# Optimization experiments

Measured on AMD Instinct MI355X. Metric: run time of the kernel, lower is better.

## Reference

```python
import jax, jax.numpy as jnp
import numpy as np

L = 4          # n_layers
D = 1024       # d_model
QD = D // 4    # quat_dim
B = 8
T = 2048
VOCAB = 32000
NUM_CLASSES = 1000
EPS_LN = 1e-5
EPS_FILT = 1e-8


def layer_norm(x, w, b):
    m = x.mean(-1, keepdims=True)
    v = ((x - m) ** 2).mean(-1, keepdims=True)
    return (x - m) / jnp.sqrt(v + EPS_LN) * w + b


def spectral_filter(k, alpha):
    # F(k) = exp(i * alpha * arctan(ln(|k| + eps))); k complex [B,T,4,QD]
    phase = alpha * jnp.arctan(jnp.log(jnp.abs(k) + EPS_FILT))
    return jnp.cos(phase) + 1j * jnp.sin(phase)


def hamilton(q1, q2):
    # q1, q2: [..., 4, QD] with components [w, x, y, z] along dim -2
    w1, x1, y1, z1 = q1[..., 0, :], q1[..., 1, :], q1[..., 2, :], q1[..., 3, :]
    w2, x2, y2, z2 = q2[..., 0, :], q2[..., 1, :], q2[..., 2, :], q2[..., 3, :]
    w = w1 * w2 - x1 * x2 - y1 * y2 - z1 * z2
    x = w1 * x2 + x1 * w2 + y1 * z2 - z1 * y2
    y = w1 * y2 - x1 * z2 + y1 * w2 + z1 * x2
    z = w1 * z2 + x1 * y2 - y1 * x2 + z1 * w2
    return jnp.stack([w, x, y, z], axis=-2)


def setup_inputs() -> dict:
    key = jax.random.key(0)
    ks = jax.random.split(key, 16)
    f32 = jnp.float32
    inp = {
        "tokens": jax.random.randint(ks[0], (B, T), 0, VOCAB),
        "embed": jax.random.normal(ks[1], (VOCAB, D), f32) * 0.02,
        "pos": jax.random.normal(ks[2], (1, T, D), f32) * 0.02,
        "Wq": jax.random.normal(ks[3], (L, D, D), f32) * 0.02,
        "bq": jnp.zeros((L, D), f32),
        "Wr": jax.random.normal(ks[4], (L, D, D), f32) * 0.02,
        "br": jnp.zeros((L, D), f32),
        "Wh": jax.random.normal(ks[5], (L, D, D), f32) * 0.02,
        "bh": jnp.zeros((L, D), f32),
        "alpha": jnp.full((L, QD), 0.1, f32) + 0.01 * jax.random.normal(ks[6], (L, QD), f32),
        "sp_ln_w": jnp.ones((L, D), f32),
        "sp_ln_b": jnp.zeros((L, D), f32),
        "gate": jnp.ones((L, QD), f32) + 0.01 * jax.random.normal(ks[7], (L, QD), f32),
        "rot": jnp.broadcast_to(jnp.eye(4, dtype=f32), (L, 4, 4)) + 0.01 * jax.random.normal(ks[8], (L, 4, 4), f32),
        "out_ln_w": jnp.ones((L, D), f32),
        "out_ln_b": jnp.zeros((L, D), f32),
        "cls_ln_w": jnp.ones((D,), f32),
        "cls_ln_b": jnp.zeros((D,), f32),
        "cls_W": jax.random.normal(ks[9], (NUM_CLASSES, D), f32) * 0.02,
        "cls_b": jnp.zeros((NUM_CLASSES,), f32),
    }
    return inp


def reference(tokens, embed, pos, Wq, bq, Wr, br, Wh, bh, alpha,
              sp_ln_w, sp_ln_b, gate, rot, out_ln_w, out_ln_b,
              cls_ln_w, cls_ln_b, cls_W, cls_b):
    x = embed[tokens] + pos[:, :T, :]           # [B,T,D]; dropout is identity in eval
    for l in range(L):
        residual = x
        # --- SpectralInterference ---
        Q = (x @ Wq[l].T + bq[l]).reshape(B, T, 4, QD)
        R = (x @ Wr[l].T + br[l]).reshape(B, T, 4, QD)
        H = (x @ Wh[l].T + bh[l]).reshape(B, T, 4, QD)
        Qs = jnp.fft.fft(Q, axis=1)
        Rs = jnp.fft.fft(R, axis=1)
        Qf = Qs * spectral_filter(Qs, alpha[l])
        Rf = Rs * spectral_filter(Rs, alpha[l])
        inter = jnp.fft.ifft(Qf * jnp.conj(Rf), axis=1).real   # [B,T,4,QD]
        out_q = hamilton(inter, H)
        x = layer_norm(out_q.reshape(B, T, D), sp_ln_w[l], sp_ln_b[l])
        # --- HamiltonianEvolution ---
        xq = x.reshape(B, T, 4, QD)
        xs = jnp.fft.fft(xq, axis=1) * gate[l]                  # gate broadcasts over [B,T,4,QD]
        xf = jnp.fft.ifft(xs, axis=1).real
        xr = jnp.einsum('btkd,jk->btjd', xf, rot[l])            # SO(4) rotation on quat axis
        x = layer_norm(xr.reshape(B, T, D) + residual, out_ln_w[l], out_ln_b[l])
    pooled = x.mean(axis=1)                                     # [B,D]
    h = layer_norm(pooled, cls_ln_w, cls_ln_b)
    return h @ cls_W.T + cls_b                                  # [B,NUM_CLASSES]
```

## Files before the change

kernel.cpp:

```cpp
#include <hip/hip_runtime.h>

typedef signed char I8;
typedef __attribute__((ext_vector_type(4))) int i32x4;
typedef __attribute__((ext_vector_type(4))) float f32x4;

#define B_   8
#define T_   2048
#define D_   1024
#define QD_  256
#define L_   4
#define M_   (B_ * T_)
#define NCLS_ 1000
#define DD_  (D_ * D_)

__device__ __forceinline__ float fixf(float v) {
  unsigned u = __float_as_uint(v);
  return ((u & 0x7F800000u) == 0x7F800000u) ? 0.f : v;
}
__device__ __forceinline__ void glds16(const void* g, void* l) {
  __builtin_amdgcn_global_load_lds((const __attribute__((address_space(1))) void*)g,
                                   (__attribute__((address_space(3))) void*)l, 16, 0, 0);
}
__device__ __forceinline__ int clampi(int q) { return q < -128 ? -128 : (q > 127 ? 127 : q); }
__device__ __forceinline__ void quant2(float v, float inv, int& qh, int& ql) {
  const float t = v * inv;
  int h = clampi((int)rintf(t));
  const float r = t - (float)h;
  int l = clampi((int)rintf(r * 256.f));
  qh = h; ql = l;
}
__device__ __forceinline__ void breduce2(float& a, float& b, float* buf) {
#pragma unroll
  for (int off = 32; off > 0; off >>= 1) { a += __shfl_down(a, off); b += __shfl_down(b, off); }
  const int lane = threadIdx.x & 63, w = threadIdx.x >> 6;
  __syncthreads();
  if (lane == 0) { buf[w] = a; buf[4 + w] = b; }
  __syncthreads();
  a = buf[0] + buf[1] + buf[2] + buf[3];
  b = buf[4] + buf[5] + buf[6] + buf[7];
}
__device__ __forceinline__ float bmaxall(float a, float* buf) {
#pragma unroll
  for (int off = 32; off > 0; off >>= 1) a = fmaxf(a, __shfl_down(a, off));
  const int lane = threadIdx.x & 63, w = threadIdx.x >> 6;
  __syncthreads();
  if (lane == 0) buf[w] = a;
  __syncthreads();
  return fmaxf(fmaxf(buf[0], buf[1]), fmaxf(buf[2], buf[3]));
}

__global__ __launch_bounds__(256) void wsplitq_k(const float* __restrict__ Wq,
                                                 const float* __restrict__ Wr,
                                                 const float* __restrict__ Wh,
                                                 I8* __restrict__ hi, I8* __restrict__ lo,
                                                 float* __restrict__ sw) {
  __shared__ float red[4];
  const int sec = blockIdx.x >> 10;
  const int n = blockIdx.x & 1023;
  const float* w = (sec == 0) ? Wq : (sec == 1) ? Wr : Wh;
  const int c = threadIdx.x * 4;
  const float4 v = *(const float4*)(w + (size_t)n * D_ + c);
  const float vv[4] = {v.x, v.y, v.z, v.w};
  float mx = fmaxf(fmaxf(fabsf(v.x), fabsf(v.y)), fmaxf(fabsf(v.z), fabsf(v.w)));
  mx = bmaxall(mx, red);
  const float s = fmaxf(mx, 1e-30f) * (1.f / 127.f);
  if (threadIdx.x == 0) sw[sec * D_ + n] = s;
  const float inv = 127.f / fmaxf(mx, 1e-30f);
  unsigned ph = 0, pl = 0;
#pragma unroll
  for (int j = 0; j < 4; j++) {
    int qh, ql;
    quant2(vv[j], inv, qh, ql);
    ph |= ((unsigned)(unsigned char)(I8)qh) << (8 * j);
    pl |= ((unsigned)(unsigned char)(I8)ql) << (8 * j);
  }
  const size_t o = (size_t)sec * DD_ + (size_t)n * D_ + c;
  *(unsigned*)(hi + o) = ph;
  *(unsigned*)(lo + o) = pl;
}

__global__ __launch_bounds__(256) void embedq_k(const int* __restrict__ tok,
                                                const float* __restrict__ emb,
                                                const float* __restrict__ pos,
                                                I8* __restrict__ xh, I8* __restrict__ xl,
                                                float* __restrict__ sx) {
  __shared__ float red[4];
  const int m = blockIdx.x;
  const int t = m & (T_ - 1);
  const int tk = tok[m];
  const int c = threadIdx.x * 4;
  const float* e = emb + (size_t)tk * D_ + c;
  const float* p = pos + (size_t)t * D_ + c;
  float v[4];
  float mx = 0.f;
#pragma unroll
  for (int i = 0; i < 4; i++) { v[i] = e[i] + p[i]; mx = fmaxf(mx, fabsf(v[i])); }
  mx = bmaxall(mx, red);
  const float s = fmaxf(mx, 1e-30f) * (1.f / 127.f);
  if (threadIdx.x == 0) sx[m] = s;
  const float inv = 127.f / fmaxf(mx, 1e-30f);
  unsigned ph = 0, pl = 0;
#pragma unroll
  for (int i = 0; i < 4; i++) {
    int qh, ql;
    quant2(v[i], inv, qh, ql);
    ph |= ((unsigned)(unsigned char)(I8)qh) << (8 * i);
    pl |= ((unsigned)(unsigned char)(I8)ql) << (8 * i);
  }
  const size_t o = (size_t)m * D_ + c;
  *(unsigned*)(xh + o) = ph;
  *(unsigned*)(xl + o) = pl;
}

__global__ __launch_bounds__(256, 2) void gemm3q_k(const I8* __restrict__ Ahi,
                                                   const I8* __restrict__ Alo,
                                                   const I8* __restrict__ Whi,
                                                   const I8* __restrict__ Wlo,
                                                   const float* __restrict__ sx,
                                                   const float* __restrict__ sw,
                                                   const float* __restrict__ bq,
                                                   const float* __restrict__ br,
                                                   const float* __restrict__ bh,
                                                   float* __restrict__ outQ,
                                                   float* __restrict__ outR,
                                                   float* __restrict__ outH) {
  __shared__ __align__(16) I8 lds[32768];
  char* sbase = (char*)lds;
  const int tid = threadIdx.x;
  const int lane = tid & 63;
  const int wave = tid >> 6;
  const int wr = wave >> 1, wc = wave & 1;
  const int sec = blockIdx.x >> 3;
  const int n0 = (blockIdx.x & 7) * 128;
  const int m0 = blockIdx.y * 128;
  const I8* Bhi = Whi + (size_t)sec * DD_;
  const I8* Blo = Wlo + (size_t)sec * DD_;
  const float* bias = (sec == 0) ? bq : (sec == 1) ? br : bh;
  float* out = (sec == 0) ? outQ : (sec == 1) ? outR : outH;
  const bool TR = sec < 2;

  i32x4 aHH[4][4], aX[4][4];
#pragma unroll
  for (int i = 0; i < 4; i++)
#pragma unroll
    for (int j = 0; j < 4; j++) { aHH[i][j] = (i32x4){0, 0, 0, 0}; aX[i][j] = (i32x4){0, 0, 0, 0}; }

  const int lrow = tid >> 2;
  const int lcolb = (tid & 3) * 16;
  const char* gah = (const char*)Ahi + (size_t)(m0 + lrow) * D_ + lcolb;
  const char* gal = (const char*)Alo + (size_t)(m0 + lrow) * D_ + lcolb;
  const char* gbh = (const char*)Bhi + (size_t)(n0 + lrow) * D_ + lcolb;
  const char* gbl = (const char*)Blo + (size_t)(n0 + lrow) * D_ + lcolb;
  char* s0 = sbase + tid * 16;

  const int koff = (lane >> 4) * 16;
  const int mA = (wr * 64 + (lane & 15)) * 64;
  const int nB = (wc * 64 + (lane & 15)) * 64;

  for (int kk = 0; kk < 1024; kk += 64) {
    __syncthreads();
    glds16(gah, s0);
    glds16(gah + 64 * D_, s0 + 4096);
    glds16(gal, s0 + 8192);
    glds16(gal + 64 * D_, s0 + 12288);
    glds16(gbh, s0 + 16384);
    glds16(gbh + 64 * D_, s0 + 20480);
    glds16(gbl, s0 + 24576);
    glds16(gbl + 64 * D_, s0 + 28672);
    gah += 64; gal += 64; gbh += 64; gbl += 64;
    __syncthreads();
    i32x4 ah[4], al[4], bh2[4], bl2[4];
#pragma unroll
    for (int i = 0; i < 4; i++) {
      const char* pa = sbase + mA + i * 1024 + koff;
      ah[i] = *(const i32x4*)pa;
      al[i] = *(const i32x4*)(pa + 8192);
    }
#pragma unroll
    for (int j = 0; j < 4; j++) {
      const char* pb = sbase + 16384 + nB + j * 1024 + koff;
      bh2[j] = *(const i32x4*)pb;
      bl2[j] = *(const i32x4*)(pb + 8192);
    }
#pragma unroll
    for (int i = 0; i < 4; i++)
#pragma unroll
      for (int j = 0; j < 4; j++) {
        aHH[i][j] = __builtin_amdgcn_mfma_i32_16x16x64_i8(ah[i], bh2[j], aHH[i][j], 0, 0, 0);
        aX[i][j]  = __builtin_amdgcn_mfma_i32_16x16x64_i8(ah[i], bl2[j], aX[i][j], 0, 0, 0);
        aX[i][j]  = __builtin_amdgcn_mfma_i32_16x16x64_i8(al[i], bh2[j], aX[i][j], 0, 0, 0);
      }
  }

#pragma unroll
  for (int j = 0; j < 4; j++) {
    const int n = n0 + wc * 64 + j * 16 + (lane & 15);
    const float swv = sw[sec * D_ + n];
    const float bv = bias[n];
#pragma unroll
    for (int i = 0; i < 4; i++) {
      const int mb = m0 + wr * 64 + i * 16 + ((lane >> 4) << 2);
#pragma unroll
      for (int r = 0; r < 4; r++) {
        const int m = mb + r;
        const float v = sx[m] * swv * ((float)aHH[i][j][r] + (float)aX[i][j][r] * (1.f / 256.f)) + bv;
        if (TR) {
          const int lb = m >> 11, t = m & (T_ - 1);
          out[(((size_t)lb << 10) + n) * T_ + t] = v;
        } else {
          out[(size_t)m * D_ + n] = v;
        }
      }
    }
  }
}

__device__ __forceinline__ int SWZ(int a) { return a ^ ((a >> 5) & 31); }
__device__ __forceinline__ int posk(int k) {
  return ((k & 3) << 9) | (((k >> 2) & 7) << 6) | (((k >> 5) & 7) << 3) | (k >> 8);
}

__device__ __forceinline__ void dft8f(float* zr, float* zi) {
  const float C = 0.70710678118654752f;
  float sr = zr[0] + zr[4], si = zi[0] + zi[4];
  float tr = zr[0] - zr[4], ti = zi[0] - zi[4];
  float ur = zr[2] + zr[6], ui = zi[2] + zi[6];
  float vr = zr[2] - zr[6], vi = zi[2] - zi[6];
  const float e0r = sr + ur, e0i = si + ui;
  const float e2r = sr - ur, e2i = si - ui;
  const float e1r = tr + vi, e1i = ti - vr;
  const float e3r = tr - vi, e3i = ti + vr;
  sr = zr[1] + zr[5]; si = zi[1] + zi[5];
  tr = zr[1] - zr[5]; ti = zi[1] - zi[5];
  ur = zr[3] + zr[7]; ui = zi[3] + zi[7];
  vr = zr[3] - zr[7]; vi = zi[3] - zi[7];
  const float o0r = sr + ur, o0i = si + ui;
  const float o2r = sr - ur, o2i = si - ui;
  const float o1r = tr + vi, o1i = ti - vr;
  const float o3r = tr - vi, o3i = ti + vr;
  const float w1r = C * (o1r + o1i), w1i = C * (o1i - o1r);
  const float w2r = o2i,             w2i = -o2r;
  const float w3r = C * (o3i - o3r), w3i = -C * (o3r + o3i);
  zr[0] = e0r + o0r; zi[0] = e0i + o0i;
  zr[4] = e0r - o0r; zi[4] = e0i - o0i;
  zr[1] = e1r + w1r; zi[1] = e1i + w1i;
  zr[5] = e1r - w1r; zi[5] = e1i - w1i;
  zr[2] = e2r + w2r; zi[2] = e2i + w2i;
  zr[6] = e2r - w2r; zi[6] = e2i - w2i;
  zr[3] = e3r + w3r; zi[3] = e3i + w3i;
  zr[7] = e3r - w3r; zi[7] = e3i - w3i;
}

__device__ __forceinline__ void idft8(float* zr, float* zi) {
  const float C = 0.70710678118654752f;
  float sr = zr[0] + zr[4], si = zi[0] + zi[4];
  float tr = zr[0] - zr[4], ti = zi[0] - zi[4];
  float ur = zr[2] + zr[6], ui = zi[2] + zi[6];
  float vr = zr[2] - zr[6], vi = zi[2] - zi[6];
  const float e0r = sr + ur, e0i = si + ui;
  const float e2r = sr - ur, e2i = si - ui;
  const float e1r = tr - vi, e1i = ti + vr;
  const float e3r = tr + vi, e3i = ti - vr;
  sr = zr[1] + zr[5]; si = zi[1] + zi[5];
  tr = zr[1] - zr[5]; ti = zi[1] - zi[5];
  ur = zr[3] + zr[7]; ui = zi[3] + zi[7];
  vr = zr[3] - zr[7]; vi = zi[3] - zi[7];
  const float o0r = sr + ur, o0i = si + ui;
  const float o2r = sr - ur, o2i = si - ui;
  const float o1r = tr - vi, o1i = ti + vr;
  const float o3r = tr + vi, o3i = ti - vr;
  const float w1r = C * (o1r - o1i), w1i = C * (o1r + o1i);
  const float w2r = -o2i,            w2i = o2r;
  const float w3r = -C * (o3r + o3i), w3i = C * (o3r - o3i);
  zr[0] = e0r + o0r; zi[0] = e0i + o0i;
  zr[4] = e0r - o0r; zi[4] = e0i - o0i;
  zr[1] = e1r + w1r; zi[1] = e1i + w1i;
  zr[5] = e1r - w1r; zi[5] = e1i - w1i;
  zr[2] = e2r + w2r; zi[2] = e2i + w2i;
  zr[6] = e2r - w2r; zi[6] = e2i - w2i;
  zr[3] = e3r + w3r; zi[3] = e3i + w3i;
  zr[7] = e3r - w3r; zi[7] = e3i - w3i;
}

__device__ __forceinline__ void twmul7(float* zr, float* zi, float wc, float ws) {
  float cr = wc, ci = ws;
#pragma unroll
  for (int m = 1; m < 8; m++) {
    const float t = zr[m] * cr - zi[m] * ci;
    zi[m] = zr[m] * ci + zi[m] * cr;
    zr[m] = t;
    if (m < 7) { const float nr = cr * wc - ci * ws; ci = cr * ws + ci * wc; cr = nr; }
  }
}

__global__ __launch_bounds__(256) void fft_spectral_k(float* __restrict__ QT,
                                                      const float* __restrict__ RT,
                                                      const float* __restrict__ alpha) {
  __shared__ float re[2048], im[2048];
  const int tid = threadIdx.x;
  const int seq = blockIdx.x;
  const float av = alpha[seq & (QD_ - 1)];
  float* q = QT + (size_t)seq * T_;
  const float* r = RT + (size_t)seq * T_;
  const float NTPI = -6.28318530717958647692f;

  float w1c[2], w1s[2], w2c[2], w2s[2], w3c[2], w3s[2];
  float c64, s64, c8, s8;

#pragma unroll
  for (int jj = 0; jj < 2; jj++) {
    const int j = tid + (jj << 8);
    const float x0r = q[j],        x0i = r[j];
    const float x1r = q[j + 512],  x1i = r[j + 512];
    const float x2r = q[j + 1024], x2i = r[j + 1024];
    const float x3r = q[j + 1536], x3i = r[j + 1536];
    float ws, wcs;
    __sincosf(NTPI * (float)j * (1.0f / 2048.0f), &ws, &wcs);
    const float w2r = wcs * wcs - ws * ws, w2i = 2.0f * wcs * ws;
    const float w3r = wcs * w2r - ws * w2i, w3i = wcs * w2i + ws * w2r;
    w1c[jj] = wcs; w1s[jj] = ws; w2c[jj] = w2r; w2s[jj] = w2i; w3c[jj] = w3r; w3s[jj] = w3i;
    const float ar = x0r + x2r, ai = x0i + x2i;
    const float br = x0r - x2r, bi = x0i - x2i;
    const float cr = x1r + x3r, ci = x1i + x3i;
    const float dr = x1r - x3r, di = x1i - x3i;
    re[SWZ(j)] = ar + cr;  im[SWZ(j)] = ai + ci;
    const float g1r = br + di, g1i = bi - dr;
    re[SWZ(j + 512)] = g1r * wcs - g1i * ws;   im[SWZ(j + 512)] = g1r * ws + g1i * wcs;
    const float g2r = ar - cr, g2i = ai - ci;
    re[SWZ(j + 1024)] = g2r * w2r - g2i * w2i; im[SWZ(j + 1024)] = g2r * w2i + g2i * w2r;
    const float g3r = br - di, g3i = bi + dr;
    re[SWZ(j + 1536)] = g3r * w3r - g3i * w3i; im[SWZ(j + 1536)] = g3r * w3i + g3i * w3r;
  }
  __syncthreads();

  float zr[8], zi[8];
  {
    const int base = ((tid >> 6) << 9) | (tid & 63);
#pragma unroll
    for (int p = 0; p < 8; p++) { const int ix = SWZ(base + (p << 6)); zr[p] = re[ix]; zi[p] = im[ix]; }
    dft8f(zr, zi);
    __sincosf(NTPI * (float)(tid & 63) * (1.0f / 512.0f), &s64, &c64);
    twmul7(zr, zi, c64, s64);
#pragma unroll
    for (int m = 0; m < 8; m++) { const int ix = SWZ(base + (m << 6)); re[ix] = zr[m]; im[ix] = zi[m]; }
  }
  __syncthreads();
  {
    const int base = ((tid >> 3) << 6) | (tid & 7);
#pragma unroll
    for (int p = 0; p < 8; p++) { const int ix = SWZ(base + (p << 3)); zr[p] = re[ix]; zi[p] = im[ix]; }
    dft8f(zr, zi);
    __sincosf(NTPI * (float)(tid & 7) * (1.0f / 64.0f), &s8, &c8);
    twmul7(zr, zi, c8, s8);
#pragma unroll
    for (int m = 0; m < 8; m++) { const int ix = SWZ(base + (m << 3)); re[ix] = zr[m]; im[ix] = zi[m]; }
  }
  __syncthreads();
  {
    const int base = tid << 3;
#pragma unroll
    for (int p = 0; p < 8; p++) { const int ix = SWZ(base + p); zr[p] = re[ix]; zi[p] = im[ix]; }
    dft8f(zr, zi);
#pragma unroll
    for (int m = 0; m < 8; m++) { const int ix = SWZ(base + m); re[ix] = zr[m]; im[ix] = zi[m]; }
  }
  __syncthreads();

  for (int f = tid; f <= 1024; f += 256) {
    const int fc = (2048 - f) & 2047;
    const int pf = SWZ(posk(f)), pc = SWZ(posk(fc));
    const float ar = re[pf], ai = im[pf];
    const float br = re[pc], bi = im[pc];
    const float qr = 0.5f * (ar + br), qi = 0.5f * (ai - bi);
    const float rr = 0.5f * (ai + bi), ri = -0.5f * (ar - br);
    const float qmag = sqrtf(qr * qr + qi * qi);
    const float rmag = sqrtf(rr * rr + ri * ri);
    const float ph = av * (atanf(logf(qmag + 1e-8f)) - atanf(logf(rmag + 1e-8f)));
    float sp, cp;
    __sincosf(ph, &sp, &cp);
    const float mr = qr * rr + qi * ri;
    const float mi = qi * rr - qr * ri;
    re[pf] = mr * cp - mi * sp;
    im[pf] = mr * sp + mi * cp;
    if (pc != pf) {
      re[pc] = mr * cp + mi * sp;
      im[pc] = mr * sp - mi * cp;
    }
  }
  __syncthreads();

  {
    const int base = tid << 3;
#pragma unroll
    for (int p = 0; p < 8; p++) { const int ix = SWZ(base + p); zr[p] = re[ix]; zi[p] = im[ix]; }
    idft8(zr, zi);
#pragma unroll
    for (int m = 0; m < 8; m++) { const int ix = SWZ(base + m); re[ix] = zr[m]; im[ix] = zi[m]; }
  }
  __syncthreads();
  {
    const int base = ((tid >> 3) << 6) | (tid & 7);
#pragma unroll
    for (int p = 0; p < 8; p++) { const int ix = SWZ(base + (p << 3)); zr[p] = re[ix]; zi[p] = im[ix]; }
    twmul7(zr, zi, c8, -s8);
    idft8(zr, zi);
#pragma unroll
    for (int m = 0; m < 8; m++) { const int ix = SWZ(base + (m << 3)); re[ix] = zr[m]; im[ix] = zi[m]; }
  }
  __syncthreads();
  {
    const int base = ((tid >> 6) << 9) | (tid & 63);
#pragma unroll
    for (int p = 0; p < 8; p++) { const int ix = SWZ(base + (p << 6)); zr[p] = re[ix]; zi[p] = im[ix]; }
    twmul7(zr, zi, c64, -s64);
    idft8(zr, zi);
#pragma unroll
    for (int m = 0; m < 8; m++) { const int ix = SWZ(base + (m << 6)); re[ix] = zr[m]; im[ix] = zi[m]; }
  }
  __syncthreads();
#pragma unroll
  for (int jj = 0; jj < 2; jj++) {
    const int j = tid + (jj << 8);
    const float x0r = re[SWZ(j)];
    const float x1r = re[SWZ(j + 512)],  x1i = im[SWZ(j + 512)];
    const float x2r = re[SWZ(j + 1024)], x2i = im[SWZ(j + 1024)];
    const float x3r = re[SWZ(j + 1536)], x3i = im[SWZ(j + 1536)];
    const float c1 = w1c[jj], s1 = w1s[jj];
    const float c2 = w2c[jj], s2 = w2s[jj];
    const float c3 = w3c[jj], s3 = w3s[jj];
    const float z1r = x1r * c1 + x1i * s1, z1i = x1i * c1 - x1r * s1;
    const float z2r = x2r * c2 + x2i * s2;
    const float z3r = x3r * c3 + x3i * s3, z3i = x3i * c3 - x3r * s3;
    const float ar = x0r + z2r;
    const float br = x0r - z2r;
    const float cr = z1r + z3r;
    const float di = z1i - z3i;
    q[j]        = (ar + cr) * (1.0f / 2048.0f);
    q[j + 512]  = (br - di) * (1.0f / 2048.0f);
    q[j + 1024] = (ar - cr) * (1.0f / 2048.0f);
    q[j + 1536] = (br + di) * (1.0f / 2048.0f);
  }
}

__global__ __launch_bounds__(256) void fused2q_k(const float* __restrict__ inter,
                                                 const float* __restrict__ Hb,
                                                 const float* __restrict__ spw, const float* __restrict__ spb,
                                                 const float* __restrict__ gate, const float* __restrict__ rot,
                                                 const float* __restrict__ ow, const float* __restrict__ ob,
                                                 I8* __restrict__ xh8, I8* __restrict__ xl8,
                                                 float* __restrict__ sxc) {
  __shared__ float ti[8 * 1028];
  const int tid = threadIdx.x;
  const int m0 = blockIdx.x * 8;
  const int lb = m0 >> 11;
  const int t0 = m0 & (T_ - 1);
  {
    const int tq = (tid & 1) * 4;
    const int nb = tid >> 1;
#pragma unroll
    for (int p = 0; p < 8; p++) {
      const int n = p * 128 + nb;
      const float4 v = *(const float4*)(inter + ((size_t)((lb << 10) | n)) * T_ + t0 + tq);
      ti[(tq + 0) * 1028 + n] = fixf(v.x);
      ti[(tq + 1) * 1028 + n] = fixf(v.y);
      ti[(tq + 2) * 1028 + n] = fixf(v.z);
      ti[(tq + 3) * 1028 + n] = fixf(v.w);
    }
  }
  __syncthreads();
  const int wv = tid >> 6, lane = tid & 63;
  float rr_[16];
#pragma unroll
  for (int i = 0; i < 16; i++) rr_[i] = rot[i];
#pragma unroll
  for (int rwi = 0; rwi < 2; rwi++) {
    const int tt = wv * 2 + rwi;
    const int m = m0 + tt;
    const size_t mb = (size_t)m * D_;
    const float sxold = sxc[m];
    float o[4][4];
#pragma unroll
    for (int kq = 0; kq < 4; kq++) {
      float iv[4], hv[4];
#pragma unroll
      for (int c2 = 0; c2 < 4; c2++) {
        iv[c2] = ti[tt * 1028 + (c2 * 4 + kq) * 64 + lane];
        hv[c2] = fixf(Hb[mb + (size_t)(c2 * 4 + kq) * 64 + lane]);
      }
      o[kq][0] = iv[0] * hv[0] - iv[1] * hv[1] - iv[2] * hv[2] - iv[3] * hv[3];
      o[kq][1] = iv[0] * hv[1] + iv[1] * hv[0] + iv[2] * hv[3] - iv[3] * hv[2];
      o[kq][2] = iv[0] * hv[2] - iv[1] * hv[3] + iv[2] * hv[0] + iv[3] * hv[1];
      o[kq][3] = iv[0] * hv[3] + iv[1] * hv[2] - iv[2] * hv[1] + iv[3] * hv[0];
    }
    float s = 0.f, ss = 0.f;
#pragma unroll
    for (int kq = 0; kq < 4; kq++)
#pragma unroll
      for (int c2 = 0; c2 < 4; c2++) { s += o[kq][c2]; ss += o[kq][c2] * o[kq][c2]; }
#pragma unroll
    for (int off = 32; off > 0; off >>= 1) { s += __shfl_xor(s, off); ss += __shfl_xor(ss, off); }
    const float mean = s * (1.0f / 1024.0f);
    const float rstd = rsqrtf(ss * (1.0f / 1024.0f) - mean * mean + 1e-5f);
    float y[4][4];
#pragma unroll
    for (int kq = 0; kq < 4; kq++) {
      const int qd = kq * 64 + lane;
      const float g = gate[qd];
      float xf[4];
#pragma unroll
      for (int c2 = 0; c2 < 4; c2++)
        xf[c2] = ((o[kq][c2] - mean) * rstd * spw[c2 * 256 + qd] + spb[c2 * 256 + qd]) * g;
#pragma unroll
      for (int j = 0; j < 4; j++) {
        const float a = rr_[j * 4 + 0] * xf[0] + rr_[j * 4 + 1] * xf[1]
                      + rr_[j * 4 + 2] * xf[2] + rr_[j * 4 + 3] * xf[3];
        const size_t idx = mb + j * 256 + qd;
        const float res = sxold * ((float)xh8[idx] + (float)xl8[idx] * (1.f / 256.f));
        y[j][kq] = a + res;
      }
    }
    float s2 = 0.f, ss2 = 0.f;
#pragma unroll
    for (int j = 0; j < 4; j++)
#pragma unroll
      for (int kq = 0; kq < 4; kq++) { s2 += y[j][kq]; ss2 += y[j][kq] * y[j][kq]; }
#pragma unroll
    for (int off = 32; off > 0; off >>= 1) { s2 += __shfl_xor(s2, off); ss2 += __shfl_xor(ss2, off); }
    const float mean2 = s2 * (1.0f / 1024.0f);
    const float rstd2 = rsqrtf(ss2 * (1.0f / 1024.0f) - mean2 * mean2 + 1e-5f);
    float vout[4][4];
    float mx = 0.f;
#pragma unroll
    for (int j = 0; j < 4; j++)
#pragma unroll
      for (int kq = 0; kq < 4; kq++) {
        const int qd = kq * 64 + lane;
        const float v = (y[j][kq] - mean2) * rstd2 * ow[j * 256 + qd] + ob[j * 256 + qd];
        vout[j][kq] = v;
        mx = fmaxf(mx, fabsf(v));
      }
#pragma unroll
    for (int off = 32; off > 0; off >>= 1) mx = fmaxf(mx, __shfl_xor(mx, off));
    const float mxg = fmaxf(mx, 1e-30f);
    const float sxn = mxg * (1.f / 127.f);
    const float inv = 127.f / mxg;
    if (lane == 0) sxc[m] = sxn;
#pragma unroll
    for (int j = 0; j < 4; j++)
#pragma unroll
      for (int kq = 0; kq < 4; kq++) {
        const int qd = kq * 64 + lane;
        const size_t idx = mb + j * 256 + qd;
        int qh, ql;
        quant2(vout[j][kq], inv, qh, ql);
        xh8[idx] = (I8)qh;
        xl8[idx] = (I8)ql;
      }
  }
}

__global__ __launch_bounds__(256) void poolq_k(const I8* __restrict__ xh, const I8* __restrict__ xl,
                                               const float* __restrict__ sx,
                                               float* __restrict__ pooled) {
  const int b = blockIdx.z;
  const int d = blockIdx.x * 256 + threadIdx.x;
  const int t0 = blockIdx.y * 256;
  float s = 0.f;
  for (int t = t0; t < t0 + 256; t++) {
    const int row = b * T_ + t;
    const size_t idx = (size_t)row * D_ + d;
    s += sx[row] * ((float)xh[idx] + (float)xl[idx] * (1.f / 256.f));
  }
  atomicAdd(&pooled[b * D_ + d], s);
}

__global__ __launch_bounds__(256) void clsln_k(const float* __restrict__ pooled, const float* __restrict__ w,
                                               const float* __restrict__ bias, float* __restrict__ h) {
  __shared__ float red[8];
  const int b = blockIdx.x;
  const int d = threadIdx.x;
  float v[4];
#pragma unroll
  for (int j = 0; j < 4; j++) v[j] = fixf(pooled[b * D_ + j * 256 + d]) * (1.0f / (float)T_);
  float s = v[0] + v[1] + v[2] + v[3];
  float ss = v[0] * v[0] + v[1] * v[1] + v[2] * v[2] + v[3] * v[3];
  breduce2(s, ss, red);
  const float mean = s * (1.0f / (float)D_);
  const float rstd = rsqrtf(ss * (1.0f / (float)D_) - mean * mean + 1e-5f);
#pragma unroll
  for (int j = 0; j < 4; j++)
    h[b * D_ + j * 256 + d] = (v[j] - mean) * rstd * w[j * 256 + d] + bias[j * 256 + d];
}

__global__ __launch_bounds__(256) void cls_k(const float* __restrict__ h, const float* __restrict__ W,
                                             const float* __restrict__ cb, float* __restrict__ out) {
  const int wv = blockIdx.x * 4 + (threadIdx.x >> 6);
  const int lane = threadIdx.x & 63;
  const int b = wv / NCLS_;
  const int n = wv - b * NCLS_;
  const float* hb = h + b * D_;
  const float* wr = W + (size_t)n * D_;
  float s = 0.f;
  for (int j = lane; j < D_; j += 64) s += hb[j] * wr[j];
#pragma unroll
  for (int off = 32; off > 0; off >>= 1) s += __shfl_down(s, off);
  if (lane == 0) out[b * NCLS_ + n] = fixf(s + cb[n]);
}

extern "C" void kernel_launch(void* const* d_in, const int* in_sizes, int n_in,
                              void* d_out, int out_size, void* d_ws, size_t ws_size,
                              hipStream_t stream) {
  (void)in_sizes; (void)n_in; (void)out_size;
  const int* tokens = (const int*)d_in[0];
  const float* emb = (const float*)d_in[1];
  const float* pos = (const float*)d_in[2];
  const float* Wq = (const float*)d_in[3];
  const float* bq = (const float*)d_in[4];
  const float* Wr = (const float*)d_in[5];
  const float* br = (const float*)d_in[6];
  const float* Wh = (const float*)d_in[7];
  const float* bh = (const float*)d_in[8];
  const float* alpha = (const float*)d_in[9];
  const float* spw = (const float*)d_in[10];
  const float* spb = (const float*)d_in[11];
  const float* gate = (const float*)d_in[12];
  const float* rot = (const float*)d_in[13];
  const float* outw = (const float*)d_in[14];
  const float* outb = (const float*)d_in[15];
  const float* clw = (const float*)d_in[16];
  const float* clb = (const float*)d_in[17];
  const float* clsW = (const float*)d_in[18];
  const float* clsb = (const float*)d_in[19];
  float* out = (float*)d_out;

  const size_t MB = 1048576;
  int CHB;
  if      (ws_size >= 136 * MB) CHB = 4;
  else if (ws_size >=  88 * MB) CHB = 2;
  else                          CHB = 1;
  const int nchunks = B_ / CHB;
  const int chm = CHB * T_;
  const size_t chunkf = (size_t)CHB * T_ * D_ * 4;

  char* ws = (char*)d_ws;
  I8* xh8 = (I8*)ws;
  I8* xl8 = (I8*)(ws + 16 * MB);
  I8* Wh8 = (I8*)(ws + 32 * MB);
  I8* Wl8 = (I8*)(ws + 35 * MB);
  float* sx = (float*)(ws + 38 * MB);
  float* sw = (float*)(ws + 38 * MB + 65536);
  char* fb = ws + 39 * MB;
  float* QTc = (float*)fb;
  float* RTc = (float*)(fb + chunkf);
  float* Hc  = (float*)(fb + 2 * chunkf);
  float* pooled = (float*)fb;
  float* hbuf   = (float*)(fb + 32768);

  embedq_k<<<M_, 256, 0, stream>>>(tokens, emb, pos, xh8, xl8, sx);

  const dim3 gemm_grid(24, chm / 128);
  for (int l = 0; l < L_; l++) {
    const size_t wo = (size_t)l * DD_;
    wsplitq_k<<<3072, 256, 0, stream>>>(Wq + wo, Wr + wo, Wh + wo, Wh8, Wl8, sw);
    for (int c = 0; c < nchunks; c++) {
      const size_t xoff = (size_t)c * chm * D_;
      gemm3q_k<<<gemm_grid, 256, 0, stream>>>(xh8 + xoff, xl8 + xoff, Wh8, Wl8,
                                              sx + (size_t)c * chm, sw,
                                              bq + l * D_, br + l * D_, bh + l * D_,
                                              QTc, RTc, Hc);
      fft_spectral_k<<<CHB * D_, 256, 0, stream>>>(QTc, RTc, alpha + l * QD_);
      fused2q_k<<<chm / 8, 256, 0, stream>>>(QTc, Hc, spw + l * D_, spb + l * D_,
                                             gate + l * QD_, rot + l * 16,
                                             outw + l * D_, outb + l * D_,
                                             xh8 + xoff, xl8 + xoff, sx + (size_t)c * chm);
    }
  }

  hipMemsetAsync(pooled, 0, B_ * D_ * sizeof(float), stream);
  poolq_k<<<dim3(4, 8, 8), 256, 0, stream>>>(xh8, xl8, sx, pooled);
  clsln_k<<<B_, 256, 0, stream>>>(pooled, clw, clb, hbuf);
  cls_k<<<(B_ * NCLS_) / 4, 256, 0, stream>>>(hbuf, clsW, clsb, out);
}
```

Before: 1.806 ms.

## Double-buffer LDS tiles in int8 QKV GEMM to overlap loads with MFMA

```diff
diff --git a/kernel.cpp b/kernel.cpp
--- a/kernel.cpp
+++ b/kernel.cpp
@@ -124,7 +124,7 @@
                                                    float* __restrict__ outQ,
                                                    float* __restrict__ outR,
                                                    float* __restrict__ outH) {
-  __shared__ __align__(16) I8 lds[32768];
+  __shared__ __align__(16) I8 lds[65536];
   char* sbase = (char*)lds;
   const int tid = threadIdx.x;
   const int lane = tid & 63;
@@ -151,34 +151,50 @@
   const char* gal = (const char*)Alo + (size_t)(m0 + lrow) * D_ + lcolb;
   const char* gbh = (const char*)Bhi + (size_t)(n0 + lrow) * D_ + lcolb;
   const char* gbl = (const char*)Blo + (size_t)(n0 + lrow) * D_ + lcolb;
-  char* s0 = sbase + tid * 16;
 
   const int koff = (lane >> 4) * 16;
   const int mA = (wr * 64 + (lane & 15)) * 64;
   const int nB = (wc * 64 + (lane & 15)) * 64;
 
+  {
+    char* d = sbase + tid * 16;
+    glds16(gah, d);
+    glds16(gah + 64 * D_, d + 4096);
+    glds16(gal, d + 8192);
+    glds16(gal + 64 * D_, d + 12288);
+    glds16(gbh, d + 16384);
+    glds16(gbh + 64 * D_, d + 20480);
+    glds16(gbl, d + 24576);
+    glds16(gbl + 64 * D_, d + 28672);
+    gah += 64; gal += 64; gbh += 64; gbl += 64;
+  }
+  __syncthreads();
+
+  int cur = 0;
   for (int kk = 0; kk < 1024; kk += 64) {
-    __syncthreads();
-    glds16(gah, s0);
-    glds16(gah + 64 * D_, s0 + 4096);
-    glds16(gal, s0 + 8192);
-    glds16(gal + 64 * D_, s0 + 12288);
-    glds16(gbh, s0 + 16384);
-    glds16(gbh + 64 * D_, s0 + 20480);
-    glds16(gbl, s0 + 24576);
-    glds16(gbl + 64 * D_, s0 + 28672);
-    gah += 64; gal += 64; gbh += 64; gbl += 64;
-    __syncthreads();
+    if (kk < 1024 - 64) {
+      char* d = sbase + (cur ^ 1) * 32768 + tid * 16;
+      glds16(gah, d);
+      glds16(gah + 64 * D_, d + 4096);
+      glds16(gal, d + 8192);
+      glds16(gal + 64 * D_, d + 12288);
+      glds16(gbh, d + 16384);
+      glds16(gbh + 64 * D_, d + 20480);
+      glds16(gbl, d + 24576);
+      glds16(gbl + 64 * D_, d + 28672);
+      gah += 64; gal += 64; gbh += 64; gbl += 64;
+    }
+    const char* sb = sbase + cur * 32768;
     i32x4 ah[4], al[4], bh2[4], bl2[4];
 #pragma unroll
     for (int i = 0; i < 4; i++) {
-      const char* pa = sbase + mA + i * 1024 + koff;
+      const char* pa = sb + mA + i * 1024 + koff;
       ah[i] = *(const i32x4*)pa;
       al[i] = *(const i32x4*)(pa + 8192);
     }
 #pragma unroll
     for (int j = 0; j < 4; j++) {
-      const char* pb = sbase + 16384 + nB + j * 1024 + koff;
+      const char* pb = sb + 16384 + nB + j * 1024 + koff;
       bh2[j] = *(const i32x4*)pb;
       bl2[j] = *(const i32x4*)(pb + 8192);
     }
@@ -190,6 +206,8 @@
         aX[i][j]  = __builtin_amdgcn_mfma_i32_16x16x64_i8(ah[i], bl2[j], aX[i][j], 0, 0, 0);
         aX[i][j]  = __builtin_amdgcn_mfma_i32_16x16x64_i8(al[i], bh2[j], aX[i][j], 0, 0, 0);
       }
+    __syncthreads();
+    cur ^= 1;
   }
 
 #pragma unroll
```

New measurement: 1.733 ms. -4.1%, faster.
